# Performance work log

Hardware: AMD Instinct MI355X
Metric: run time of the kernel (lower is better)

Reference implementation:

```python
import jax, jax.numpy as jnp
import numpy as np

NUM_GRAPHS = 64
NODE_SZ = 200
FEAT = 200
HID = 256          # hidden_size; each signed branch outputs HID//2
HALF = HID // 2
N_NODES = NUM_GRAPHS * NODE_SZ
N_EDGES = 409600
NUM_LAYERS = 3


def _lin_init(key, out_f, in_f):
    kw, kb = jax.random.split(key)
    s = 1.0 / np.sqrt(in_f)
    W = jax.random.uniform(kw, (out_f, in_f), minval=-s, maxval=s, dtype=jnp.float32)
    b = jax.random.uniform(kb, (out_f,), minval=-s, maxval=s, dtype=jnp.float32)
    return W, b


def setup_inputs() -> dict:
    key = jax.random.key(0)
    ks = jax.random.split(key, 16)
    x = jax.random.normal(ks[0], (N_NODES, FEAT), dtype=jnp.float32)
    edge_index = jax.random.randint(ks[1], (2, N_EDGES), 0, N_NODES, dtype=jnp.int64)
    edge_weight = jax.random.normal(ks[2], (N_EDGES,), dtype=jnp.float32)
    batch = jnp.repeat(jnp.arange(NUM_GRAPHS, dtype=jnp.int64), NODE_SZ)

    # signed conv layer params: layer0 in=FEAT, layers 1..: in=HID; each lin maps 2*in -> HALF
    Wp0, bp0 = _lin_init(ks[3], HALF, 2 * FEAT)
    Wn0, bn0 = _lin_init(ks[4], HALF, 2 * FEAT)
    Wp1, bp1 = _lin_init(ks[5], HALF, 2 * HID)
    Wn1, bn1 = _lin_init(ks[6], HALF, 2 * HID)
    Wp2, bp2 = _lin_init(ks[7], HALF, 2 * HID)
    Wn2, bn2 = _lin_init(ks[8], HALF, 2 * HID)
    Wr, br = _lin_init(ks[9], HID, NODE_SZ * HID)   # readout_lin
    Wl, bl = _lin_init(ks[10], 1, HID)              # final lin
    return dict(x=x, edge_index=edge_index, edge_weight=edge_weight, batch=batch,
                Wp0=Wp0, bp0=bp0, Wn0=Wn0, bn0=bn0,
                Wp1=Wp1, bp1=bp1, Wn1=Wn1, bn1=bn1,
                Wp2=Wp2, bp2=bp2, Wn2=Wn2, bn2=bn2,
                Wr=Wr, br=br, Wl=Wl, bl=bl)


def _signed_conv(x, src, dst, w, Wp, bp, Wn, bn):
    # edge-weighted signed mean aggregation, split by weight sign
    xs = x[src]                                   # [E, D] gather
    pw = jnp.where(w > 0, w, 0.0)
    nw = jnp.where(w < 0, -w, 0.0)
    agg_p = jax.ops.segment_sum(pw[:, None] * xs, dst, num_segments=N_NODES)
    agg_n = jax.ops.segment_sum(nw[:, None] * xs, dst, num_segments=N_NODES)
    deg_p = jax.ops.segment_sum((w > 0).astype(x.dtype), dst, num_segments=N_NODES)
    deg_n = jax.ops.segment_sum((w < 0).astype(x.dtype), dst, num_segments=N_NODES)
    agg_p = agg_p / jnp.maximum(deg_p, 1.0)[:, None]
    agg_n = agg_n / jnp.maximum(deg_n, 1.0)[:, None]
    hp = jnp.concatenate([agg_p, x], -1) @ Wp.T + bp
    hn = jnp.concatenate([agg_n, x], -1) @ Wn.T + bn
    return jnp.concatenate([hp, hn], -1)          # [N, HID]


def reference(x, edge_index, edge_weight, batch,
              Wp0, bp0, Wn0, bn0, Wp1, bp1, Wn1, bn1, Wp2, bp2, Wn2, bn2,
              Wr, br, Wl, bl):
    src, dst = edge_index[0], edge_index[1]
    convs = [(Wp0, bp0, Wn0, bn0), (Wp1, bp1, Wn1, bn1), (Wp2, bp2, Wn2, bn2)]
    h = x
    for i, (Wp, bp, Wn, bn) in enumerate(convs):
        h = _signed_conv(h, src, dst, edge_weight, Wp, bp, Wn, bn)
        if i < NUM_LAYERS - 1:
            h = jax.nn.leaky_relu(h, negative_slope=0.01)
    # per-graph readout: batch is contiguous with NODE_SZ nodes per graph,
    # so the boolean-mask+view loop is exactly a reshape.
    g = h.reshape(NUM_GRAPHS, NODE_SZ * HID)
    g = g @ Wr.T + br                             # [G, HID]
    # dropout(p=0.5) is identity in eval mode
    return g @ Wl.T + bl                          # [G, 1]
```

## Files before the change

kernel.cpp:

```cpp
#include <hip/hip_runtime.h>

#define NUM_GRAPHS 64
#define NODE_SZ    200
#define FEAT       200
#define HID        256
#define HALF       128
#define N_NODES    (NUM_GRAPHS * NODE_SZ)
#define KREAD      (NODE_SZ * HID)

typedef unsigned short ushort_t;
typedef unsigned int uint_t;
typedef __attribute__((ext_vector_type(8))) short bf16x8;
typedef __attribute__((ext_vector_type(4))) float f32x4;

#define GAS(p) ((const __attribute__((address_space(1))) void*)(p))
#define LAS(p) ((__attribute__((address_space(3))) void*)(p))

__device__ __forceinline__ float bf2f(ushort_t u) {
    union { unsigned int i; float f; } v; v.i = ((unsigned int)u) << 16; return v.f;
}
__device__ __forceinline__ ushort_t f2bf(float f) {
    union { float f; unsigned int i; } v; v.f = f;
    unsigned int x = v.i;
    unsigned int r = (x + 0x7fffu + ((x >> 16) & 1u)) >> 16;
    return (ushort_t)r;
}

#define OFF_CNT    0
#define OFF_WEFF   51264
#define OFF_ES     256064
#define OFF_YALL   13363264
#define OFF_HA     26470464
#define OFF_HB     33024064
#define OFF_WALL   39577664
#define OFF_XB     40364096

__global__ __launch_bounds__(256) void prep_kernel(
        const float* __restrict__ Wp0, const float* __restrict__ Wn0,
        const float* __restrict__ Wp1, const float* __restrict__ Wn1,
        const float* __restrict__ Wp2, const float* __restrict__ Wn2,
        const float* __restrict__ x, const float* __restrict__ Wr,
        const float* __restrict__ Wl, const float* __restrict__ br,
        const float* __restrict__ bl,
        ushort_t* __restrict__ wall, ushort_t* __restrict__ xb,
        float* __restrict__ weff, float* __restrict__ outg) {
    int bx = blockIdx.x, tid = threadIdx.x;
    if (bx < 200) {
        int k = bx * 256 + tid;
        float s[16];
#pragma unroll
        for (int j = 0; j < 16; ++j) s[j] = 0.f;
#pragma unroll 1
        for (int c = 0; c < 256; c += 16) {
#pragma unroll
            for (int j = 0; j < 16; ++j)
                s[j] = fmaf(Wl[c + j], Wr[(size_t)(c + j) * KREAD + k], s[j]);
        }
        float t0 = ((s[0] + s[1]) + (s[2] + s[3])) + ((s[4] + s[5]) + (s[6] + s[7]));
        float t1 = ((s[8] + s[9]) + (s[10] + s[11])) + ((s[12] + s[13]) + (s[14] + s[15]));
        weff[k] = t0 + t1;
    } else if (bx < 300) {
        for (int idx = (bx - 200) * 256 + tid; idx < N_NODES * 64; idx += 25600) {
            int n = idx >> 6, c0 = (idx & 63) * 4;
            ushort4 o = {0, 0, 0, 0};
            if (c0 < 200) {
                float4 v = *(const float4*)&x[(size_t)n * 200 + c0];
                o.x = f2bf(v.x); o.y = f2bf(v.y); o.z = f2bf(v.z); o.w = f2bf(v.w);
            }
            *(ushort4*)&xb[(size_t)n * 256 + c0] = o;
        }
    } else if (bx < 364) {
        for (int idx = (bx - 300) * 256 + tid; idx < 3 * 131072; idx += 16384) {
            int layer = idx >> 17, within = idx & 131071;
            int rr = within >> 8, col = within & 255;
            const float* Wp = (layer == 0) ? Wp0 : (layer == 1) ? Wp1 : Wp2;
            const float* Wn = (layer == 0) ? Wn0 : (layer == 1) ? Wn1 : Wn2;
            int Ks = (layer == 0) ? 200 : 256;
            int q = rr >> 7;
            const float* Wsrc = (q & 1) ? Wn : Wp;
            int row = rr & 127;
            int scol = col + ((q >> 1) ? Ks : 0);
            float v = (col < Ks) ? Wsrc[(size_t)row * (2 * Ks) + scol] : 0.0f;
            wall[idx] = f2bf(v);
        }
    } else {
        if (tid < 64) {
            float p = br[tid] * Wl[tid] + br[tid + 64] * Wl[tid + 64]
                    + br[tid + 128] * Wl[tid + 128] + br[tid + 192] * Wl[tid + 192];
#pragma unroll
            for (int d = 32; d > 0; d >>= 1) p += __shfl_xor(p, d);
            outg[tid] = p + bl[0];
        }
    }
}

__device__ __forceinline__ void gemm_body(int t, const ushort_t* __restrict__ A,
                                          const ushort_t* __restrict__ Bw,
                                          ushort_t* __restrict__ Y,
                                          ushort_t* smem) {
    int mBase = (t >> 1) * 128;
    int nBase = (t & 1) * 256;
    int tid  = threadIdx.x;
    int lane = tid & 63;
    int wv   = tid >> 6;
    int r    = lane & 15;
    int quad = lane >> 4;
    int wm   = wv >> 1;
    int wn   = wv & 1;

    int rowA = tid >> 2, colc = (tid & 3) * 8;
    const ushort_t* gA  = A  + (size_t)(mBase + rowA) * 256 + colc;
    const ushort_t* gB0 = Bw + (size_t)(nBase + rowA) * 256 + colc;
    const ushort_t* gB1 = Bw + (size_t)(nBase + 128 + rowA) * 256 + colc;

    f32x4 acc[2][8];
#pragma unroll
    for (int i = 0; i < 2; ++i)
#pragma unroll
        for (int j = 0; j < 8; ++j) acc[i][j] = (f32x4){0.f, 0.f, 0.f, 0.f};

    auto STAGE = [&](int buf, int kb) {
        ushort_t* Ad = smem + (buf << 12) + tid * 8;
        ushort_t* Bd = smem + 8192 + (buf << 13) + tid * 8;
        __builtin_amdgcn_global_load_lds(GAS(gA + kb), LAS(Ad), 16, 0, 0);
        __builtin_amdgcn_global_load_lds(GAS(gB0 + kb), LAS(Bd), 16, 0, 0);
        __builtin_amdgcn_global_load_lds(GAS(gB1 + kb), LAS(Bd + 4096), 16, 0, 0);
    };

    STAGE(0, 0);
    for (int kt = 0; kt < 8; ++kt) {
        int cb = kt & 1;
        __syncthreads();
        if (kt < 7) STAGE(cb ^ 1, (kt + 1) * 32);
        const ushort_t* Ac = smem + (cb << 12);
        const ushort_t* Bc = smem + 8192 + (cb << 13);
        bf16x8 af[2];
#pragma unroll
        for (int i = 0; i < 2; ++i)
            af[i] = *(const bf16x8*)&Ac[(wm * 32 + i * 16 + r) * 32 + quad * 8];
#pragma unroll
        for (int j = 0; j < 8; ++j) {
            bf16x8 bfr = *(const bf16x8*)&Bc[(wn * 128 + j * 16 + r) * 32 + quad * 8];
            acc[0][j] = __builtin_amdgcn_mfma_f32_16x16x32_bf16(af[0], bfr, acc[0][j], 0, 0, 0);
            acc[1][j] = __builtin_amdgcn_mfma_f32_16x16x32_bf16(af[1], bfr, acc[1][j], 0, 0, 0);
        }
    }
#pragma unroll
    for (int i = 0; i < 2; ++i)
#pragma unroll
        for (int j = 0; j < 8; ++j) {
            int c = nBase + wn * 128 + j * 16 + r;
#pragma unroll
            for (int reg = 0; reg < 4; ++reg) {
                int m = mBase + wm * 32 + i * 16 + quad * 4 + reg;
                Y[(size_t)m * 512 + c] = f2bf(acc[i][j][reg]);
            }
        }
}

__global__ __launch_bounds__(512) void scatgemm_kernel(
        const int* __restrict__ ei, const float* __restrict__ ew,
        uint_t* __restrict__ cnt, uint2* __restrict__ es, int E,
        const ushort_t* __restrict__ xb, const ushort_t* __restrict__ wall,
        ushort_t* __restrict__ Yall) {
    __shared__ __align__(16) ushort_t smem[24576];
    int bx = blockIdx.x;
    if (bx < 200) {
        gemm_body(bx, xb, wall, Yall, smem);
        return;
    }
    int e = (bx - 200) * 512 + threadIdx.x;
    if (e < E) {
        int src = ei[e];
        int dst = ei[E + e];
        float w = ew[e];
        if (w > 0.0f) {
            uint_t old = atomicAdd(&cnt[dst], 1u);
            uint_t rk = old & 0xffffu;
            if (rk < 64u)
                es[(size_t)dst * 128 + rk] = make_uint2((uint_t)src, __float_as_uint(w));
        } else if (w < 0.0f) {
            uint_t old = atomicAdd(&cnt[dst], 0x10000u);
            uint_t rk = old >> 16;
            if (rk < 64u)
                es[(size_t)dst * 128 + 64 + rk] = make_uint2((uint_t)src, __float_as_uint(-w));
        }
    }
}

__global__ __launch_bounds__(512) void gemm_kernel(const ushort_t* __restrict__ A,
                                                   const ushort_t* __restrict__ Bw,
                                                   ushort_t* __restrict__ Y) {
    __shared__ __align__(16) ushort_t smem[24576];
    gemm_body(blockIdx.x, A, Bw, Y, smem);
}

template <bool LEAKY, bool DOT>
__global__ __launch_bounds__(256) void agg_kernel(
        const ushort_t* __restrict__ Y,
        const uint_t* __restrict__ cnt,
        const uint2* __restrict__ es,
        const float* __restrict__ bp, const float* __restrict__ bn,
        ushort_t* __restrict__ outp,
        const float* __restrict__ weff,
        float* __restrict__ outg) {
    __shared__ float sdot[4];
    int lane = threadIdx.x & 63;
    int wv   = threadIdx.x >> 6;
    int n = blockIdx.x * 4 + wv;
    int half = lane >> 5;
    int hl   = lane & 31;
    int c0   = hl * 4;
    uint_t c = __builtin_amdgcn_readfirstlane(cnt[n]);
    uint_t kp = c & 0xffffu, kn = c >> 16;
    uint_t kh = half ? kn : kp;
    uint_t himax = max(kp, kn);

    const uint2* esb = es + (size_t)n * 128 + (half ? 64 : 0);
    const ushort_t* Yph = Y + half * 128 + c0;

    float acc[4] = {0.f, 0.f, 0.f, 0.f};
    uint_t clampi = (kh > 0u) ? (kh - 1u) : 0u;

#pragma unroll 1
    for (uint_t e = 0; e < himax; e += 8) {
        uint2 u[8];
        float w[8];
#pragma unroll
        for (int j = 0; j < 8; ++j) {
            uint_t idx = e + (uint_t)j;
            uint2 r = esb[min(idx, clampi)];
            w[j] = (idx < kh) ? __uint_as_float(r.y) : 0.0f;
            uint_t s = min(r.x, (uint_t)(N_NODES - 1));
            u[j] = *(const uint2*)&Yph[(size_t)s * 512];
        }
#pragma unroll
        for (int j = 0; j < 8; ++j) {
            const ushort_t* q = (const ushort_t*)&u[j];
            acc[0] = fmaf(w[j], bf2f(q[0]), acc[0]);
            acc[1] = fmaf(w[j], bf2f(q[1]), acc[1]);
            acc[2] = fmaf(w[j], bf2f(q[2]), acc[2]);
            acc[3] = fmaf(w[j], bf2f(q[3]), acc[3]);
        }
    }

    float d = fmaxf((float)kh, 1.0f);
    float rcp = 1.0f / d;
    uint2 z = *(const uint2*)&Y[(size_t)n * 512 + 256 + half * 128 + c0];
    const ushort_t* zq = (const ushort_t*)&z;
    const float* bb = half ? bn : bp;
    float4 bv = *(const float4*)&bb[c0];
    float v0 = fmaf(acc[0], rcp, bf2f(zq[0]) + bv.x);
    float v1 = fmaf(acc[1], rcp, bf2f(zq[1]) + bv.y);
    float v2 = fmaf(acc[2], rcp, bf2f(zq[2]) + bv.z);
    float v3 = fmaf(acc[3], rcp, bf2f(zq[3]) + bv.w);
    if (LEAKY) {
        v0 = (v0 > 0.0f) ? v0 : 0.01f * v0;
        v1 = (v1 > 0.0f) ? v1 : 0.01f * v1;
        v2 = (v2 > 0.0f) ? v2 : 0.01f * v2;
        v3 = (v3 > 0.0f) ? v3 : 0.01f * v3;
    }
    if (DOT) {
        int g = blockIdx.x / 50;
        int kbase = (n % 200) * 256 + half * 128 + c0;
        float4 wf = *(const float4*)&weff[kbase];
        float s = v0 * wf.x + v1 * wf.y + v2 * wf.z + v3 * wf.w;
#pragma unroll
        for (int dd = 32; dd > 0; dd >>= 1) s += __shfl_xor(s, dd);
        if (lane == 0) sdot[wv] = s;
        __syncthreads();
        if (threadIdx.x == 0)
            atomicAdd(&outg[g], (sdot[0] + sdot[1]) + (sdot[2] + sdot[3]));
    } else {
        uint2 o;
        o.x = (uint_t)f2bf(v0) | ((uint_t)f2bf(v1) << 16);
        o.y = (uint_t)f2bf(v2) | ((uint_t)f2bf(v3) << 16);
        *(uint2*)&outp[(size_t)n * 256 + half * 128 + c0] = o;
    }
}

extern "C" void kernel_launch(void* const* d_in, const int* in_sizes, int n_in,
                              void* d_out, int out_size, void* d_ws, size_t ws_size,
                              hipStream_t stream) {
    const float* x  = (const float*)d_in[0];
    const int*   ei = (const int*)d_in[1];
    const float* ew = (const float*)d_in[2];
    const float* Wp0 = (const float*)d_in[4];
    const float* bp0 = (const float*)d_in[5];
    const float* Wn0 = (const float*)d_in[6];
    const float* bn0 = (const float*)d_in[7];
    const float* Wp1 = (const float*)d_in[8];
    const float* bp1 = (const float*)d_in[9];
    const float* Wn1 = (const float*)d_in[10];
    const float* bn1 = (const float*)d_in[11];
    const float* Wp2 = (const float*)d_in[12];
    const float* bp2 = (const float*)d_in[13];
    const float* Wn2 = (const float*)d_in[14];
    const float* bn2 = (const float*)d_in[15];
    const float* Wr  = (const float*)d_in[16];
    const float* br  = (const float*)d_in[17];
    const float* Wl  = (const float*)d_in[18];
    const float* bl  = (const float*)d_in[19];
    const int E = in_sizes[1] / 2;

    char* ws = (char*)d_ws;
    uint_t*   cnt    = (uint_t*)(ws + OFF_CNT);
    float*    weff   = (float*)(ws + OFF_WEFF);
    uint2*    es     = (uint2*)(ws + OFF_ES);
    ushort_t* Yall   = (ushort_t*)(ws + OFF_YALL);
    ushort_t* hA     = (ushort_t*)(ws + OFF_HA);
    ushort_t* hB     = (ushort_t*)(ws + OFF_HB);
    ushort_t* wall   = (ushort_t*)(ws + OFF_WALL);
    ushort_t* xb     = (ushort_t*)(ws + OFF_XB);
    float*    outg   = (float*)d_out;

    hipMemsetAsync(ws + OFF_CNT, 0, N_NODES * sizeof(uint_t), stream);
    hipLaunchKernelGGL(prep_kernel, dim3(365), dim3(256), 0, stream,
                       Wp0, Wn0, Wp1, Wn1, Wp2, Wn2, x, Wr, Wl, br, bl,
                       wall, xb, weff, outg);
    hipLaunchKernelGGL(scatgemm_kernel, dim3(200 + (E + 511) / 512), dim3(512), 0, stream,
                       ei, ew, cnt, es, E, xb, wall, Yall);
    hipLaunchKernelGGL((agg_kernel<true, false>), dim3(N_NODES / 4), dim3(256), 0, stream,
                       Yall, cnt, es, bp0, bn0, hA, (const float*)nullptr, (float*)nullptr);
    hipLaunchKernelGGL(gemm_kernel, dim3(200), dim3(512), 0, stream, hA, wall + 131072, Yall);
    hipLaunchKernelGGL((agg_kernel<true, false>), dim3(N_NODES / 4), dim3(256), 0, stream,
                       Yall, cnt, es, bp1, bn1, hB, (const float*)nullptr, (float*)nullptr);
    hipLaunchKernelGGL(gemm_kernel, dim3(200), dim3(512), 0, stream, hB, wall + 262144, Yall);
    hipLaunchKernelGGL((agg_kernel<false, true>), dim3(N_NODES / 4), dim3(256), 0, stream,
                       Yall, cnt, es, bp2, bn2, (ushort_t*)nullptr, weff, outg);
}
```

Measured before the change: 293.3 us.

## Split aggregation across sign and column slices for finer per-thread work

Replaces the per-node aggregation in the first two layers with a sliced kernel where each block handles 8 nodes and one of four sign/column-half slices, and each thread gathers 2 columns instead of 4. The goal is more blocks and more independent loads in flight, so each wave gathers edges for one sign and avoids idling when positive and negative degrees differ. Edge metadata is now reread four times per node and each gather is a narrower 4-byte load. The final dot-product layer keeps the old per-node structure.

```diff
diff --git a/kernel.cpp b/kernel.cpp
--- a/kernel.cpp
+++ b/kernel.cpp
@@ -195,13 +195,71 @@
     gemm_body(blockIdx.x, A, Bw, Y, smem);
 }
 
-template <bool LEAKY, bool DOT>
-__global__ __launch_bounds__(256) void agg_kernel(
+template <bool LEAKY>
+__global__ __launch_bounds__(256) void agg_slice_kernel(
         const ushort_t* __restrict__ Y,
         const uint_t* __restrict__ cnt,
         const uint2* __restrict__ es,
         const float* __restrict__ bp, const float* __restrict__ bn,
-        ushort_t* __restrict__ outp,
+        ushort_t* __restrict__ outp) {
+    int b = blockIdx.x;
+    int s = b & 3;
+    int sign = s >> 1;
+    int ch   = (s & 1) * 64;
+    int nodeBase = (b >> 2) * 8;
+    int tid = threadIdx.x;
+    int wv = tid >> 6;
+    int half = (tid >> 5) & 1;
+    int hl = tid & 31;
+    int n = nodeBase + wv * 2 + half;
+    int col = ch + hl * 2;
+    int gcol = sign * 128 + col;
+
+    uint_t c = cnt[n];
+    uint_t kh = sign ? (c >> 16) : (c & 0xffffu);
+    const uint2* esb = es + (size_t)n * 128 + sign * 64;
+    const ushort_t* Yg = Y + gcol;
+
+    float acc0 = 0.f, acc1 = 0.f;
+    uint_t clampi = kh ? kh - 1u : 0u;
+
+#pragma unroll 1
+    for (uint_t e = 0; e < kh; e += 8) {
+        uint_t u[8];
+        float w[8];
+#pragma unroll
+        for (int j = 0; j < 8; ++j) {
+            uint_t idx = e + (uint_t)j;
+            uint2 r = esb[min(idx, clampi)];
+            w[j] = (idx < kh) ? __uint_as_float(r.y) : 0.0f;
+            uint_t src = min(r.x, (uint_t)(N_NODES - 1));
+            u[j] = *(const uint_t*)&Yg[(size_t)src * 512];
+        }
+#pragma unroll
+        for (int j = 0; j < 8; ++j) {
+            acc0 = fmaf(w[j], bf2f((ushort_t)(u[j] & 0xffffu)), acc0);
+            acc1 = fmaf(w[j], bf2f((ushort_t)(u[j] >> 16)), acc1);
+        }
+    }
+
+    float rcp = 1.0f / fmaxf((float)kh, 1.0f);
+    uint_t z = *(const uint_t*)&Y[(size_t)n * 512 + 256 + gcol];
+    const float* bb = sign ? bn : bp;
+    float v0 = fmaf(acc0, rcp, bf2f((ushort_t)(z & 0xffffu)) + bb[col]);
+    float v1 = fmaf(acc1, rcp, bf2f((ushort_t)(z >> 16))     + bb[col + 1]);
+    if (LEAKY) {
+        v0 = (v0 > 0.0f) ? v0 : 0.01f * v0;
+        v1 = (v1 > 0.0f) ? v1 : 0.01f * v1;
+    }
+    uint_t o = (uint_t)f2bf(v0) | ((uint_t)f2bf(v1) << 16);
+    *(uint_t*)&outp[(size_t)n * 256 + gcol] = o;
+}
+
+__global__ __launch_bounds__(256) void agg_dot_kernel(
+        const ushort_t* __restrict__ Y,
+        const uint_t* __restrict__ cnt,
+        const uint2* __restrict__ es,
+        const float* __restrict__ bp, const float* __restrict__ bn,
         const float* __restrict__ weff,
         float* __restrict__ outg) {
     __shared__ float sdot[4];
@@ -254,29 +312,16 @@
     float v1 = fmaf(acc[1], rcp, bf2f(zq[1]) + bv.y);
     float v2 = fmaf(acc[2], rcp, bf2f(zq[2]) + bv.z);
     float v3 = fmaf(acc[3], rcp, bf2f(zq[3]) + bv.w);
-    if (LEAKY) {
-        v0 = (v0 > 0.0f) ? v0 : 0.01f * v0;
-        v1 = (v1 > 0.0f) ? v1 : 0.01f * v1;
-        v2 = (v2 > 0.0f) ? v2 : 0.01f * v2;
-        v3 = (v3 > 0.0f) ? v3 : 0.01f * v3;
-    }
-    if (DOT) {
-        int g = blockIdx.x / 50;
-        int kbase = (n % 200) * 256 + half * 128 + c0;
-        float4 wf = *(const float4*)&weff[kbase];
-        float s = v0 * wf.x + v1 * wf.y + v2 * wf.z + v3 * wf.w;
-#pragma unroll
-        for (int dd = 32; dd > 0; dd >>= 1) s += __shfl_xor(s, dd);
-        if (lane == 0) sdot[wv] = s;
-        __syncthreads();
-        if (threadIdx.x == 0)
-            atomicAdd(&outg[g], (sdot[0] + sdot[1]) + (sdot[2] + sdot[3]));
-    } else {
-        uint2 o;
-        o.x = (uint_t)f2bf(v0) | ((uint_t)f2bf(v1) << 16);
-        o.y = (uint_t)f2bf(v2) | ((uint_t)f2bf(v3) << 16);
-        *(uint2*)&outp[(size_t)n * 256 + half * 128 + c0] = o;
-    }
+    int g = blockIdx.x / 50;
+    int kbase = (n % 200) * 256 + half * 128 + c0;
+    float4 wf = *(const float4*)&weff[kbase];
+    float s = v0 * wf.x + v1 * wf.y + v2 * wf.z + v3 * wf.w;
+#pragma unroll
+    for (int dd = 32; dd > 0; dd >>= 1) s += __shfl_xor(s, dd);
+    if (lane == 0) sdot[wv] = s;
+    __syncthreads();
+    if (threadIdx.x == 0)
+        atomicAdd(&outg[g], (sdot[0] + sdot[1]) + (sdot[2] + sdot[3]));
 }
 
 extern "C" void kernel_launch(void* const* d_in, const int* in_sizes, int n_in,
@@ -320,12 +365,12 @@
                        wall, xb, weff, outg);
     hipLaunchKernelGGL(scatgemm_kernel, dim3(200 + (E + 511) / 512), dim3(512), 0, stream,
                        ei, ew, cnt, es, E, xb, wall, Yall);
-    hipLaunchKernelGGL((agg_kernel<true, false>), dim3(N_NODES / 4), dim3(256), 0, stream,
-                       Yall, cnt, es, bp0, bn0, hA, (const float*)nullptr, (float*)nullptr);
+    hipLaunchKernelGGL((agg_slice_kernel<true>), dim3(N_NODES / 8 * 4), dim3(256), 0, stream,
+                       Yall, cnt, es, bp0, bn0, hA);
     hipLaunchKernelGGL(gemm_kernel, dim3(200), dim3(512), 0, stream, hA, wall + 131072, Yall);
-    hipLaunchKernelGGL((agg_kernel<true, false>), dim3(N_NODES / 4), dim3(256), 0, stream,
-                       Yall, cnt, es, bp1, bn1, hB, (const float*)nullptr, (float*)nullptr);
+    hipLaunchKernelGGL((agg_slice_kernel<true>), dim3(N_NODES / 8 * 4), dim3(256), 0, stream,
+                       Yall, cnt, es, bp1, bn1, hB);
     hipLaunchKernelGGL(gemm_kernel, dim3(200), dim3(512), 0, stream, hB, wall + 262144, Yall);
-    hipLaunchKernelGGL((agg_kernel<false, true>), dim3(N_NODES / 4), dim3(256), 0, stream,
-                       Yall, cnt, es, bp2, bn2, (ushort_t*)nullptr, weff, outg);
-}
+    hipLaunchKernelGGL(agg_dot_kernel, dim3(N_NODES / 4), dim3(256), 0, stream,
+                       Yall, cnt, es, bp2, bn2, weff, outg);
+}
```

Measured after the change: 309.3 us. 1.05x slower.
